# Kernel optimization log

Hardware: AMD Instinct MI355X
Metric: run time of the kernel (lower is better)

## Reference

```python
import jax, jax.numpy as jnp
import numpy as np
import math

D_MODEL = 1024
N_HEADS = 16
D_K = D_MODEL // N_HEADS


def setup_inputs() -> dict:
    key = jax.random.key(0)
    ks = jax.random.split(key, 12)
    B, S, D = 4, 2048, D_MODEL
    scale = 1.0 / math.sqrt(D)
    inp = {
        "q": jax.random.normal(ks[0], (B, S, D), jnp.float32),
        "k": jax.random.normal(ks[1], (B, S, D), jnp.float32),
        "v": jax.random.normal(ks[2], (B, S, D), jnp.float32),
        "w_q": jax.random.normal(ks[3], (D, D), jnp.float32) * scale,
        "b_q": jnp.zeros((D,), jnp.float32),
        "w_k": jax.random.normal(ks[4], (D, D), jnp.float32) * scale,
        "b_k": jnp.zeros((D,), jnp.float32),
        "w_v": jax.random.normal(ks[5], (D, D), jnp.float32) * scale,
        "b_v": jnp.zeros((D,), jnp.float32),
        "w_o": jax.random.normal(ks[6], (D, D), jnp.float32) * scale,
        "b_o": jnp.zeros((D,), jnp.float32),
        "ln_gamma": jnp.ones((D,), jnp.float32),
        "ln_beta": jnp.zeros((D,), jnp.float32),
    }
    return inp


def reference(q, k, v, w_q, b_q, w_k, b_k, w_v, b_v, w_o, b_o, ln_gamma, ln_beta):
    B, Sq, D = q.shape
    Sk = k.shape[1]
    residual = q
    # Projections (torch Linear: x @ W.T + b); split into heads -> [B, H, S, d_k]
    qh = (q @ w_q.T + b_q).reshape(B, Sq, N_HEADS, D_K).transpose(0, 2, 1, 3)
    kh = (k @ w_k.T + b_k).reshape(B, Sk, N_HEADS, D_K).transpose(0, 2, 1, 3)
    vh = (v @ w_v.T + b_v).reshape(B, Sk, N_HEADS, D_K).transpose(0, 2, 1, 3)
    # Scaled dot-product attention (dropout is identity in eval mode)
    scores = jnp.einsum("bhqd,bhkd->bhqk", qh, kh) / jnp.sqrt(jnp.float32(D_K))
    attn = jax.nn.softmax(scores, axis=-1)  # [B, H, Sq, Sk]
    ctx = jnp.einsum("bhqk,bhkd->bhqd", attn, vh)
    ctx = ctx.transpose(0, 2, 1, 3).reshape(B, Sq, D)
    out = ctx @ w_o.T + b_o
    # Post-LN with residual
    x = out + residual
    mu = jnp.mean(x, axis=-1, keepdims=True)
    var = jnp.var(x, axis=-1, keepdims=True)
    out = (x - mu) / jnp.sqrt(var + 1e-5) * ln_gamma + ln_beta
    return out, attn
```

## Files before the change

### kernel.cpp

```cpp
#include <hip/hip_runtime.h>

#define B_ 4
#define S_ 2048
#define D_ 1024
#define H_ 16
#define DK_ 64
#define M_ (B_ * S_)

typedef __attribute__((ext_vector_type(8))) _Float16 f16x8;
typedef __attribute__((ext_vector_type(4))) _Float16 f16x4;
typedef __attribute__((ext_vector_type(4))) float f32x4;

#define QSCALE 0.18033688011113607f

__device__ __forceinline__ f32x4 mfma16(f16x8 a, f16x8 b, f32x4 c) {
  return __builtin_amdgcn_mfma_f32_16x16x32_f16(a, b, c, 0, 0, 0);
}

__device__ __forceinline__ void gl2lds(const _Float16* g, _Float16* l) {
  __builtin_amdgcn_global_load_lds(
      (const __attribute__((address_space(1))) void*)g,
      (__attribute__((address_space(3))) void*)l, 16, 0, 0);
}

#define NW8 (D_ * D_ / 8)
__global__ __launch_bounds__(256) void cvt_w(
    const float* __restrict__ wq, const float* __restrict__ wk,
    const float* __restrict__ wv, const float* __restrict__ wo,
    _Float16* __restrict__ wqh, _Float16* __restrict__ wkh,
    _Float16* __restrict__ wvh, _Float16* __restrict__ woh) {
  const int i = blockIdx.x * 256 + threadIdx.x;
  const int t = i >> 17;
  const int off = i & (NW8 - 1);
  const float* src = t == 0 ? wq : (t == 1 ? wk : (t == 2 ? wv : wo));
  _Float16* dst = t == 0 ? wqh : (t == 1 ? wkh : (t == 2 ? wvh : woh));
  const f32x4 a = *reinterpret_cast<const f32x4*>(&src[(size_t)off * 8]);
  const f32x4 b = *reinterpret_cast<const f32x4*>(&src[(size_t)off * 8 + 4]);
  f16x8 h;
  h[0] = (_Float16)a[0]; h[1] = (_Float16)a[1]; h[2] = (_Float16)a[2]; h[3] = (_Float16)a[3];
  h[4] = (_Float16)b[0]; h[5] = (_Float16)b[1]; h[6] = (_Float16)b[2]; h[7] = (_Float16)b[3];
  *reinterpret_cast<f16x8*>(&dst[(size_t)off * 8]) = h;
}

__global__ __launch_bounds__(256) void gemm_qkv(
    const float* __restrict__ Xq, const float* __restrict__ Xk, const float* __restrict__ Xv,
    const _Float16* __restrict__ Wq, const _Float16* __restrict__ Wk, const _Float16* __restrict__ Wv,
    const float* __restrict__ bq, const float* __restrict__ bk, const float* __restrict__ bv,
    _Float16* __restrict__ Qh, _Float16* __restrict__ Kh, _Float16* __restrict__ Vt) {
  __shared__ _Float16 As[128 * 72];
  __shared__ _Float16 Bs[128 * 64];
  const int third = blockIdx.x >> 9;
  const int bid = blockIdx.x & 511;
  const float* X = third == 0 ? Xq : (third == 1 ? Xk : Xv);
  const _Float16* Bw = third == 0 ? Wq : (third == 1 ? Wk : Wv);
  const float* bias = third == 0 ? bq : (third == 1 ? bk : bv);

  const int t = threadIdx.x;
  const int lane = t & 63;
  const int w = t >> 6;
  const int wr = w >> 1, wc = w & 1;
  const int l15 = lane & 15, g = lane >> 4;
  const int m0 = (bid & 63) * 128;
  const int n0 = (bid >> 6) * 128;

  f32x4 acc[4][4] = {};
  const int srow = lane >> 3;
  const int schk = (lane & 7) * 8;
  const int ar = t >> 4;
  const int ac = (t & 15) * 4;

  for (int kt = 0; kt < 16; ++kt) {
    const int k0 = kt * 64;
#pragma unroll
    for (int u = 0; u < 4; ++u)
      gl2lds(&Bw[(size_t)(n0 + u * 32 + w * 8 + srow) * D_ + k0 + schk], &Bs[u * 2048 + w * 512]);
#pragma unroll
    for (int rg = 0; rg < 8; ++rg) {
      const int r = rg * 16 + ar;
      const f32x4 vv = *reinterpret_cast<const f32x4*>(&X[(size_t)(m0 + r) * D_ + k0 + ac]);
      f16x4 hh;
      hh[0] = (_Float16)vv[0]; hh[1] = (_Float16)vv[1];
      hh[2] = (_Float16)vv[2]; hh[3] = (_Float16)vv[3];
      *reinterpret_cast<f16x4*>(&As[r * 72 + ac]) = hh;
    }
    __syncthreads();
#pragma unroll
    for (int kk = 0; kk < 2; ++kk) {
      f16x8 af[4], bfr[4];
#pragma unroll
      for (int m = 0; m < 4; ++m)
        af[m] = *reinterpret_cast<const f16x8*>(&As[(wr * 64 + m * 16 + l15) * 72 + kk * 32 + 8 * g]);
#pragma unroll
      for (int n = 0; n < 4; ++n)
        bfr[n] = *reinterpret_cast<const f16x8*>(&Bs[(wc * 64 + n * 16 + l15) * 64 + kk * 32 + 8 * g]);
#pragma unroll
      for (int m = 0; m < 4; ++m)
#pragma unroll
        for (int n = 0; n < 4; ++n)
          acc[m][n] = mfma16(af[m], bfr[n], acc[m][n]);
    }
    __syncthreads();
  }

  if (third < 2) {
    _Float16* Y = third == 0 ? Qh : Kh;
    const float scl = third == 0 ? QSCALE : 1.0f;
#pragma unroll
    for (int m = 0; m < 4; ++m)
#pragma unroll
      for (int n = 0; n < 4; ++n)
#pragma unroll
        for (int i = 0; i < 4; ++i) {
          const int R = m0 + wr * 64 + m * 16 + 4 * g + i;
          const int C = n0 + wc * 64 + n * 16 + l15;
          Y[(size_t)R * D_ + C] = (_Float16)((acc[m][n][i] + bias[C]) * scl);
        }
  } else {
#pragma unroll
    for (int m = 0; m < 4; ++m)
#pragma unroll
      for (int n = 0; n < 4; ++n) {
        const int R0 = m0 + wr * 64 + m * 16 + 4 * g;
        const int C = n0 + wc * 64 + n * 16 + l15;
        const int b = R0 >> 11, s0 = R0 & (S_ - 1);
        const int h = C >> 6, dk = C & (DK_ - 1);
        f16x4 hv;
#pragma unroll
        for (int i = 0; i < 4; ++i) hv[i] = (_Float16)(acc[m][n][i] + bias[C]);
        *reinterpret_cast<f16x4*>(&Vt[((size_t)((b * H_ + h) * DK_ + dk)) * S_ + s0]) = hv;
      }
  }
}

__global__ __launch_bounds__(256) void gemm_out(const _Float16* __restrict__ A,
                                                const _Float16* __restrict__ Bw,
                                                const float* __restrict__ bias,
                                                float* __restrict__ out) {
  __shared__ _Float16 As[128 * 64];
  __shared__ _Float16 Bs[128 * 64];
  const int t = threadIdx.x;
  const int lane = t & 63;
  const int w = t >> 6;
  const int wr = w >> 1, wc = w & 1;
  const int l15 = lane & 15, g = lane >> 4;
  const int m0 = (blockIdx.x & 63) * 128;
  const int n0 = (blockIdx.x >> 6) * 128;

  f32x4 acc[4][4] = {};
  const int srow = lane >> 3;
  const int schk = (lane & 7) * 8;

  for (int kt = 0; kt < 16; ++kt) {
    const int k0 = kt * 64;
#pragma unroll
    for (int u = 0; u < 4; ++u) {
      const int r = u * 32 + w * 8 + srow;
      gl2lds(&A[(size_t)(m0 + r) * D_ + k0 + schk], &As[u * 2048 + w * 512]);
      gl2lds(&Bw[(size_t)(n0 + r) * D_ + k0 + schk], &Bs[u * 2048 + w * 512]);
    }
    __syncthreads();
#pragma unroll
    for (int kk = 0; kk < 2; ++kk) {
      f16x8 af[4], bfr[4];
#pragma unroll
      for (int m = 0; m < 4; ++m)
        af[m] = *reinterpret_cast<const f16x8*>(&As[(wr * 64 + m * 16 + l15) * 64 + kk * 32 + 8 * g]);
#pragma unroll
      for (int n = 0; n < 4; ++n)
        bfr[n] = *reinterpret_cast<const f16x8*>(&Bs[(wc * 64 + n * 16 + l15) * 64 + kk * 32 + 8 * g]);
#pragma unroll
      for (int m = 0; m < 4; ++m)
#pragma unroll
        for (int n = 0; n < 4; ++n)
          acc[m][n] = mfma16(af[m], bfr[n], acc[m][n]);
    }
    __syncthreads();
  }

#pragma unroll
  for (int m = 0; m < 4; ++m)
#pragma unroll
    for (int n = 0; n < 4; ++n)
#pragma unroll
      for (int i = 0; i < 4; ++i) {
        const int R = m0 + wr * 64 + m * 16 + 4 * g + i;
        const int C = n0 + wc * 64 + n * 16 + l15;
        out[(size_t)R * D_ + C] = acc[m][n][i] + bias[C];
      }
}

__global__ __launch_bounds__(256) void attn_pass1(const _Float16* __restrict__ Qh,
                                                  const _Float16* __restrict__ Kh,
                                                  float* __restrict__ lbuf) {
  __shared__ float red[4][64];
  const int t = threadIdx.x;
  const int lane = t & 63;
  const int w = t >> 6;
  const int l15 = lane & 15, g = lane >> 4;
  const int qc = blockIdx.x & 31;
  const int bh = blockIdx.x >> 5;
  const int b = bh >> 4, h = bh & 15;
  const int q0 = qc * 64;
  const _Float16* Qp = Qh + (size_t)b * S_ * D_ + h * DK_;
  const _Float16* Kp = Kh + (size_t)b * S_ * D_ + h * DK_;

  f16x8 qa[4][2];
#pragma unroll
  for (int mr = 0; mr < 4; ++mr)
#pragma unroll
    for (int kk = 0; kk < 2; ++kk)
      qa[mr][kk] = *reinterpret_cast<const f16x8*>(&Qp[(size_t)(q0 + mr * 16 + l15) * D_ + kk * 32 + 8 * g]);

  float l[4][4] = {};
  const int cbeg = w * (S_ / 4), cend = cbeg + (S_ / 4);
  for (int c0 = cbeg; c0 < cend; c0 += 16) {
    const f16x8 kb0 = *reinterpret_cast<const f16x8*>(&Kp[(size_t)(c0 + l15) * D_ + 8 * g]);
    const f16x8 kb1 = *reinterpret_cast<const f16x8*>(&Kp[(size_t)(c0 + l15) * D_ + 32 + 8 * g]);
#pragma unroll
    for (int mr = 0; mr < 4; ++mr) {
      f32x4 sc = {};
      sc = mfma16(qa[mr][0], kb0, sc);
      sc = mfma16(qa[mr][1], kb1, sc);
#pragma unroll
      for (int i = 0; i < 4; ++i) l[mr][i] += exp2f(sc[i]);
    }
  }
#pragma unroll
  for (int mask = 1; mask < 16; mask <<= 1)
#pragma unroll
    for (int mr = 0; mr < 4; ++mr)
#pragma unroll
      for (int i = 0; i < 4; ++i) l[mr][i] += __shfl_xor(l[mr][i], mask, 64);
  if (l15 == 0)
#pragma unroll
    for (int mr = 0; mr < 4; ++mr)
#pragma unroll
      for (int i = 0; i < 4; ++i) red[w][mr * 16 + 4 * g + i] = l[mr][i];
  __syncthreads();
  if (t < 64)
    lbuf[(size_t)bh * S_ + q0 + t] = red[0][t] + red[1][t] + red[2][t] + red[3][t];
}

__global__ __launch_bounds__(256) void attn_pass2(const _Float16* __restrict__ Qh,
                                                  const _Float16* __restrict__ Kh,
                                                  const _Float16* __restrict__ Vt,
                                                  const float* __restrict__ lbuf,
                                                  float* __restrict__ attn,
                                                  _Float16* __restrict__ ctx) {
  __shared__ float Ps[4][32 * 36];
  const int t = threadIdx.x;
  const int lane = t & 63;
  const int w = t >> 6;
  const int l15 = lane & 15, g = lane >> 4;
  const int qc = blockIdx.x & 15;
  const int bh = blockIdx.x >> 4;
  const int b = bh >> 4, h = bh & 15;
  const int q0 = qc * 128 + w * 32;
  const _Float16* Qp = Qh + (size_t)b * S_ * D_ + h * DK_;
  const _Float16* Kp = Kh + (size_t)b * S_ * D_ + h * DK_;
  const _Float16* Vp = Vt + (size_t)bh * DK_ * S_;

  f16x8 qa[2][2];
#pragma unroll
  for (int mr = 0; mr < 2; ++mr)
#pragma unroll
    for (int kk = 0; kk < 2; ++kk)
      qa[mr][kk] = *reinterpret_cast<const f16x8*>(&Qp[(size_t)(q0 + mr * 16 + l15) * D_ + kk * 32 + 8 * g]);

  float il[2][4];
#pragma unroll
  for (int mr = 0; mr < 2; ++mr)
#pragma unroll
    for (int i = 0; i < 4; ++i)
      il[mr][i] = 1.0f / lbuf[(size_t)bh * S_ + q0 + mr * 16 + 4 * g + i];

  f32x4 accv[2][4] = {};
  float* Pw = Ps[w];
  const int sr = lane >> 3;
  const int sc4 = (lane & 7) * 4;

  for (int c0 = 0; c0 < S_; c0 += 32) {
#pragma unroll
    for (int ct = 0; ct < 2; ++ct) {
      const f16x8 kb0 = *reinterpret_cast<const f16x8*>(&Kp[(size_t)(c0 + ct * 16 + l15) * D_ + 8 * g]);
      const f16x8 kb1 = *reinterpret_cast<const f16x8*>(&Kp[(size_t)(c0 + ct * 16 + l15) * D_ + 32 + 8 * g]);
#pragma unroll
      for (int mr = 0; mr < 2; ++mr) {
        f32x4 sc = {};
        sc = mfma16(qa[mr][0], kb0, sc);
        sc = mfma16(qa[mr][1], kb1, sc);
#pragma unroll
        for (int i = 0; i < 4; ++i)
          Pw[(mr * 16 + 4 * g + i) * 36 + ct * 16 + l15] = exp2f(sc[i]) * il[mr][i];
      }
    }
#pragma unroll
    for (int j = 0; j < 4; ++j) {
      const int r = sr + 8 * j;
      const f32x4 pv = *reinterpret_cast<const f32x4*>(&Pw[r * 36 + sc4]);
      __builtin_nontemporal_store(pv,
          reinterpret_cast<f32x4*>(&attn[((size_t)bh * S_ + q0 + r) * S_ + c0 + sc4]));
    }
#pragma unroll
    for (int mr = 0; mr < 2; ++mr) {
      const f32x4 p0 = *reinterpret_cast<const f32x4*>(&Pw[(mr * 16 + l15) * 36 + 8 * g]);
      const f32x4 p1 = *reinterpret_cast<const f32x4*>(&Pw[(mr * 16 + l15) * 36 + 8 * g + 4]);
      f16x8 pa;
#pragma unroll
      for (int j = 0; j < 4; ++j) { pa[j] = (_Float16)p0[j]; pa[4 + j] = (_Float16)p1[j]; }
#pragma unroll
      for (int n = 0; n < 4; ++n) {
        const f16x8 vb = *reinterpret_cast<const f16x8*>(&Vp[(size_t)(n * 16 + l15) * S_ + c0 + 8 * g]);
        accv[mr][n] = mfma16(pa, vb, accv[mr][n]);
      }
    }
  }
#pragma unroll
  for (int mr = 0; mr < 2; ++mr)
#pragma unroll
    for (int n = 0; n < 4; ++n)
#pragma unroll
      for (int i = 0; i < 4; ++i) {
        const int row = q0 + mr * 16 + 4 * g + i;
        ctx[((size_t)(b * S_ + row)) * D_ + h * DK_ + n * 16 + l15] = (_Float16)accv[mr][n][i];
      }
}

__global__ __launch_bounds__(256) void ln_kernel(float* __restrict__ out,
                                                 const float* __restrict__ resid,
                                                 const float* __restrict__ gamma,
                                                 const float* __restrict__ beta) {
  __shared__ float red[8];
  const int row = blockIdx.x;
  const int t = threadIdx.x;
  const int lane = t & 63, w = t >> 6;
  const size_t base = (size_t)row * D_ + t * 4;
  const f32x4 o = *reinterpret_cast<const f32x4*>(&out[base]);
  const f32x4 r = *reinterpret_cast<const f32x4*>(&resid[base]);
  const f32x4 x = o + r;
  float s = x[0] + x[1] + x[2] + x[3];
  float s2 = x[0] * x[0] + x[1] * x[1] + x[2] * x[2] + x[3] * x[3];
#pragma unroll
  for (int mask = 1; mask < 64; mask <<= 1) {
    s += __shfl_xor(s, mask, 64);
    s2 += __shfl_xor(s2, mask, 64);
  }
  if (lane == 0) { red[w] = s; red[w + 4] = s2; }
  __syncthreads();
  s = red[0] + red[1] + red[2] + red[3];
  s2 = red[4] + red[5] + red[6] + red[7];
  const float mu = s * (1.0f / D_);
  const float var = s2 * (1.0f / D_) - mu * mu;
  const float rstd = rsqrtf(var + 1e-5f);
  const f32x4 gm = *reinterpret_cast<const f32x4*>(&gamma[t * 4]);
  const f32x4 bt = *reinterpret_cast<const f32x4*>(&beta[t * 4]);
  f32x4 y;
#pragma unroll
  for (int j = 0; j < 4; ++j) y[j] = (x[j] - mu) * rstd * gm[j] + bt[j];
  *reinterpret_cast<f32x4*>(&out[base]) = y;
}

extern "C" void kernel_launch(void* const* d_in, const int* in_sizes, int n_in,
                              void* d_out, int out_size, void* d_ws, size_t ws_size,
                              hipStream_t stream) {
  (void)in_sizes; (void)n_in; (void)out_size; (void)ws_size;
  const float* q    = (const float*)d_in[0];
  const float* k    = (const float*)d_in[1];
  const float* v    = (const float*)d_in[2];
  const float* w_q  = (const float*)d_in[3];
  const float* b_q  = (const float*)d_in[4];
  const float* w_k  = (const float*)d_in[5];
  const float* b_k  = (const float*)d_in[6];
  const float* w_v  = (const float*)d_in[7];
  const float* b_v  = (const float*)d_in[8];
  const float* w_o  = (const float*)d_in[9];
  const float* b_o  = (const float*)d_in[10];
  const float* ln_g = (const float*)d_in[11];
  const float* ln_b = (const float*)d_in[12];

  char* ws = (char*)d_ws;
  _Float16* wq_h = (_Float16*)(ws + ((size_t)0 << 20));
  _Float16* wk_h = (_Float16*)(ws + ((size_t)2 << 20));
  _Float16* wv_h = (_Float16*)(ws + ((size_t)4 << 20));
  _Float16* wo_h = (_Float16*)(ws + ((size_t)6 << 20));
  _Float16* Qh   = (_Float16*)(ws + ((size_t)8 << 20));
  _Float16* Kh   = (_Float16*)(ws + ((size_t)26 << 20));
  _Float16* Vt   = (_Float16*)(ws + ((size_t)44 << 20));
  _Float16* ctx  = (_Float16*)(ws + ((size_t)62 << 20));
  float*    lbuf = (float*)(ws + ((size_t)80 << 20));

  float* out_f = (float*)d_out;
  float* attn_f = out_f + (size_t)M_ * D_;

  cvt_w<<<4 * NW8 / 256, 256, 0, stream>>>(w_q, w_k, w_v, w_o, wq_h, wk_h, wv_h, wo_h);

  gemm_qkv<<<1536, 256, 0, stream>>>(q, k, v, wq_h, wk_h, wv_h, b_q, b_k, b_v, Qh, Kh, Vt);

  attn_pass1<<<B_ * H_ * (S_ / 64), 256, 0, stream>>>(Qh, Kh, lbuf);
  attn_pass2<<<B_ * H_ * (S_ / 128), 256, 0, stream>>>(Qh, Kh, Vt, lbuf, attn_f, ctx);

  gemm_out<<<512, 256, 0, stream>>>(ctx, wo_h, b_o, out_f);
  ln_kernel<<<M_, 256, 0, stream>>>(out_f, q, ln_g, ln_b);
}
```

Baseline: 509.5 us.

## Pre-convert activations to fp16 and use 32x32 MFMA in attention pass 2

The cvt kernel now also converts q, k and v to fp16 ahead of time, so the QKV GEMM can stream both operands into LDS with direct global-to-LDS loads instead of converting fp32 in registers. Attention pass 2 switches from 16x16x32 to 32x32x16 MFMA tiles for both QK^T and PV, which needs fewer instructions and reloads fewer K/V fragments. The cost is an extra full fp32 read and fp16 write of the inputs. The A tile in LDS also loses its row padding, which may introduce bank conflicts.

```diff
diff --git a/kernel.cpp b/kernel.cpp
--- a/kernel.cpp
+++ b/kernel.cpp
@@ -10,11 +10,15 @@
 typedef __attribute__((ext_vector_type(8))) _Float16 f16x8;
 typedef __attribute__((ext_vector_type(4))) _Float16 f16x4;
 typedef __attribute__((ext_vector_type(4))) float f32x4;
+typedef __attribute__((ext_vector_type(16))) float f32x16;
 
 #define QSCALE 0.18033688011113607f
 
 __device__ __forceinline__ f32x4 mfma16(f16x8 a, f16x8 b, f32x4 c) {
   return __builtin_amdgcn_mfma_f32_16x16x32_f16(a, b, c, 0, 0, 0);
+}
+__device__ __forceinline__ f32x16 mfma32(f16x8 a, f16x8 b, f32x16 c) {
+  return __builtin_amdgcn_mfma_f32_32x32x16_f16(a, b, c, 0, 0, 0);
 }
 
 __device__ __forceinline__ void gl2lds(const _Float16* g, _Float16* l) {
@@ -23,17 +27,31 @@
       (__attribute__((address_space(3))) void*)l, 16, 0, 0);
 }
 
+#define NIN8 (M_ * D_ / 8)
 #define NW8 (D_ * D_ / 8)
-__global__ __launch_bounds__(256) void cvt_w(
-    const float* __restrict__ wq, const float* __restrict__ wk,
-    const float* __restrict__ wv, const float* __restrict__ wo,
-    _Float16* __restrict__ wqh, _Float16* __restrict__ wkh,
-    _Float16* __restrict__ wvh, _Float16* __restrict__ woh) {
+__global__ __launch_bounds__(256) void cvt_all(
+    const float* __restrict__ q, const float* __restrict__ k, const float* __restrict__ v,
+    const float* __restrict__ wq, const float* __restrict__ wk, const float* __restrict__ wv,
+    const float* __restrict__ wo,
+    _Float16* __restrict__ qf, _Float16* __restrict__ kf, _Float16* __restrict__ vf,
+    _Float16* __restrict__ wqh, _Float16* __restrict__ wkh, _Float16* __restrict__ wvh,
+    _Float16* __restrict__ woh) {
   const int i = blockIdx.x * 256 + threadIdx.x;
-  const int t = i >> 17;
-  const int off = i & (NW8 - 1);
-  const float* src = t == 0 ? wq : (t == 1 ? wk : (t == 2 ? wv : wo));
-  _Float16* dst = t == 0 ? wqh : (t == 1 ? wkh : (t == 2 ? wvh : woh));
+  const float* src;
+  _Float16* dst;
+  int off;
+  if (i < 3 * NIN8) {
+    const int t = i >> 20;
+    off = i & (NIN8 - 1);
+    src = t == 0 ? q : (t == 1 ? k : v);
+    dst = t == 0 ? qf : (t == 1 ? kf : vf);
+  } else {
+    const int j = i - 3 * NIN8;
+    const int t = j >> 17;
+    off = j & (NW8 - 1);
+    src = t == 0 ? wq : (t == 1 ? wk : (t == 2 ? wv : wo));
+    dst = t == 0 ? wqh : (t == 1 ? wkh : (t == 2 ? wvh : woh));
+  }
   const f32x4 a = *reinterpret_cast<const f32x4*>(&src[(size_t)off * 8]);
   const f32x4 b = *reinterpret_cast<const f32x4*>(&src[(size_t)off * 8 + 4]);
   f16x8 h;
@@ -43,15 +61,15 @@
 }
 
 __global__ __launch_bounds__(256) void gemm_qkv(
-    const float* __restrict__ Xq, const float* __restrict__ Xk, const float* __restrict__ Xv,
+    const _Float16* __restrict__ Aq, const _Float16* __restrict__ Ak, const _Float16* __restrict__ Av,
     const _Float16* __restrict__ Wq, const _Float16* __restrict__ Wk, const _Float16* __restrict__ Wv,
     const float* __restrict__ bq, const float* __restrict__ bk, const float* __restrict__ bv,
     _Float16* __restrict__ Qh, _Float16* __restrict__ Kh, _Float16* __restrict__ Vt) {
-  __shared__ _Float16 As[128 * 72];
+  __shared__ _Float16 As[128 * 64];
   __shared__ _Float16 Bs[128 * 64];
   const int third = blockIdx.x >> 9;
   const int bid = blockIdx.x & 511;
-  const float* X = third == 0 ? Xq : (third == 1 ? Xk : Xv);
+  const _Float16* A = third == 0 ? Aq : (third == 1 ? Ak : Av);
   const _Float16* Bw = third == 0 ? Wq : (third == 1 ? Wk : Wv);
   const float* bias = third == 0 ? bq : (third == 1 ? bk : bv);
 
@@ -66,22 +84,14 @@
   f32x4 acc[4][4] = {};
   const int srow = lane >> 3;
   const int schk = (lane & 7) * 8;
-  const int ar = t >> 4;
-  const int ac = (t & 15) * 4;
 
   for (int kt = 0; kt < 16; ++kt) {
     const int k0 = kt * 64;
 #pragma unroll
-    for (int u = 0; u < 4; ++u)
-      gl2lds(&Bw[(size_t)(n0 + u * 32 + w * 8 + srow) * D_ + k0 + schk], &Bs[u * 2048 + w * 512]);
-#pragma unroll
-    for (int rg = 0; rg < 8; ++rg) {
-      const int r = rg * 16 + ar;
-      const f32x4 vv = *reinterpret_cast<const f32x4*>(&X[(size_t)(m0 + r) * D_ + k0 + ac]);
-      f16x4 hh;
-      hh[0] = (_Float16)vv[0]; hh[1] = (_Float16)vv[1];
-      hh[2] = (_Float16)vv[2]; hh[3] = (_Float16)vv[3];
-      *reinterpret_cast<f16x4*>(&As[r * 72 + ac]) = hh;
+    for (int u = 0; u < 4; ++u) {
+      const int r = u * 32 + w * 8 + srow;
+      gl2lds(&A[(size_t)(m0 + r) * D_ + k0 + schk], &As[u * 2048 + w * 512]);
+      gl2lds(&Bw[(size_t)(n0 + r) * D_ + k0 + schk], &Bs[u * 2048 + w * 512]);
     }
     __syncthreads();
 #pragma unroll
@@ -89,7 +99,7 @@
       f16x8 af[4], bfr[4];
 #pragma unroll
       for (int m = 0; m < 4; ++m)
-        af[m] = *reinterpret_cast<const f16x8*>(&As[(wr * 64 + m * 16 + l15) * 72 + kk * 32 + 8 * g]);
+        af[m] = *reinterpret_cast<const f16x8*>(&As[(wr * 64 + m * 16 + l15) * 64 + kk * 32 + 8 * g]);
 #pragma unroll
       for (int n = 0; n < 4; ++n)
         bfr[n] = *reinterpret_cast<const f16x8*>(&Bs[(wc * 64 + n * 16 + l15) * 64 + kk * 32 + 8 * g]);
@@ -251,7 +261,7 @@
   const int t = threadIdx.x;
   const int lane = t & 63;
   const int w = t >> 6;
-  const int l15 = lane & 15, g = lane >> 4;
+  const int l31 = lane & 31, hs = lane >> 5;
   const int qc = blockIdx.x & 15;
   const int bh = blockIdx.x >> 4;
   const int b = bh >> 4, h = bh & 15;
@@ -260,70 +270,59 @@
   const _Float16* Kp = Kh + (size_t)b * S_ * D_ + h * DK_;
   const _Float16* Vp = Vt + (size_t)bh * DK_ * S_;
 
-  f16x8 qa[2][2];
-#pragma unroll
-  for (int mr = 0; mr < 2; ++mr)
-#pragma unroll
-    for (int kk = 0; kk < 2; ++kk)
-      qa[mr][kk] = *reinterpret_cast<const f16x8*>(&Qp[(size_t)(q0 + mr * 16 + l15) * D_ + kk * 32 + 8 * g]);
-
-  float il[2][4];
-#pragma unroll
-  for (int mr = 0; mr < 2; ++mr)
-#pragma unroll
-    for (int i = 0; i < 4; ++i)
-      il[mr][i] = 1.0f / lbuf[(size_t)bh * S_ + q0 + mr * 16 + 4 * g + i];
-
-  f32x4 accv[2][4] = {};
+  f16x8 qa[4];
+#pragma unroll
+  for (int kc = 0; kc < 4; ++kc)
+    qa[kc] = *reinterpret_cast<const f16x8*>(&Qp[(size_t)(q0 + l31) * D_ + kc * 16 + 8 * hs]);
+
+  float il[16];
+#pragma unroll
+  for (int r = 0; r < 16; ++r)
+    il[r] = 1.0f / lbuf[(size_t)bh * S_ + q0 + (r & 3) + 8 * (r >> 2) + 4 * hs];
+
+  f32x16 pv0 = {}, pv1 = {};
   float* Pw = Ps[w];
   const int sr = lane >> 3;
   const int sc4 = (lane & 7) * 4;
 
   for (int c0 = 0; c0 < S_; c0 += 32) {
-#pragma unroll
-    for (int ct = 0; ct < 2; ++ct) {
-      const f16x8 kb0 = *reinterpret_cast<const f16x8*>(&Kp[(size_t)(c0 + ct * 16 + l15) * D_ + 8 * g]);
-      const f16x8 kb1 = *reinterpret_cast<const f16x8*>(&Kp[(size_t)(c0 + ct * 16 + l15) * D_ + 32 + 8 * g]);
-#pragma unroll
-      for (int mr = 0; mr < 2; ++mr) {
-        f32x4 sc = {};
-        sc = mfma16(qa[mr][0], kb0, sc);
-        sc = mfma16(qa[mr][1], kb1, sc);
-#pragma unroll
-        for (int i = 0; i < 4; ++i)
-          Pw[(mr * 16 + 4 * g + i) * 36 + ct * 16 + l15] = exp2f(sc[i]) * il[mr][i];
-      }
-    }
+    f32x16 sc = {};
+#pragma unroll
+    for (int kc = 0; kc < 4; ++kc) {
+      const f16x8 kb = *reinterpret_cast<const f16x8*>(&Kp[(size_t)(c0 + l31) * D_ + kc * 16 + 8 * hs]);
+      sc = mfma32(qa[kc], kb, sc);
+    }
+#pragma unroll
+    for (int r = 0; r < 16; ++r)
+      Pw[((r & 3) + 8 * (r >> 2) + 4 * hs) * 36 + l31] = exp2f(sc[r]) * il[r];
 #pragma unroll
     for (int j = 0; j < 4; ++j) {
       const int r = sr + 8 * j;
-      const f32x4 pv = *reinterpret_cast<const f32x4*>(&Pw[r * 36 + sc4]);
-      __builtin_nontemporal_store(pv,
+      const f32x4 pvv = *reinterpret_cast<const f32x4*>(&Pw[r * 36 + sc4]);
+      __builtin_nontemporal_store(pvv,
           reinterpret_cast<f32x4*>(&attn[((size_t)bh * S_ + q0 + r) * S_ + c0 + sc4]));
     }
 #pragma unroll
-    for (int mr = 0; mr < 2; ++mr) {
-      const f32x4 p0 = *reinterpret_cast<const f32x4*>(&Pw[(mr * 16 + l15) * 36 + 8 * g]);
-      const f32x4 p1 = *reinterpret_cast<const f32x4*>(&Pw[(mr * 16 + l15) * 36 + 8 * g + 4]);
+    for (int kc2 = 0; kc2 < 2; ++kc2) {
+      const int cb = kc2 * 16 + 8 * hs;
+      const f32x4 p0 = *reinterpret_cast<const f32x4*>(&Pw[l31 * 36 + cb]);
+      const f32x4 p1 = *reinterpret_cast<const f32x4*>(&Pw[l31 * 36 + cb + 4]);
       f16x8 pa;
 #pragma unroll
-      for (int j = 0; j < 4; ++j) { pa[j] = (_Float16)p0[j]; pa[4 + j] = (_Float16)p1[j]; }
-#pragma unroll
-      for (int n = 0; n < 4; ++n) {
-        const f16x8 vb = *reinterpret_cast<const f16x8*>(&Vp[(size_t)(n * 16 + l15) * S_ + c0 + 8 * g]);
-        accv[mr][n] = mfma16(pa, vb, accv[mr][n]);
-      }
-    }
-  }
-#pragma unroll
-  for (int mr = 0; mr < 2; ++mr)
-#pragma unroll
-    for (int n = 0; n < 4; ++n)
-#pragma unroll
-      for (int i = 0; i < 4; ++i) {
-        const int row = q0 + mr * 16 + 4 * g + i;
-        ctx[((size_t)(b * S_ + row)) * D_ + h * DK_ + n * 16 + l15] = (_Float16)accv[mr][n][i];
-      }
+      for (int jj = 0; jj < 4; ++jj) { pa[jj] = (_Float16)p0[jj]; pa[4 + jj] = (_Float16)p1[jj]; }
+      const f16x8 vb0 = *reinterpret_cast<const f16x8*>(&Vp[(size_t)(0 * 32 + l31) * S_ + c0 + cb]);
+      const f16x8 vb1 = *reinterpret_cast<const f16x8*>(&Vp[(size_t)(1 * 32 + l31) * S_ + c0 + cb]);
+      pv0 = mfma32(pa, vb0, pv0);
+      pv1 = mfma32(pa, vb1, pv1);
+    }
+  }
+#pragma unroll
+  for (int r = 0; r < 16; ++r) {
+    const int row = q0 + (r & 3) + 8 * (r >> 2) + 4 * hs;
+    _Float16* cp = &ctx[((size_t)(b * S_ + row)) * D_ + h * DK_];
+    cp[l31] = (_Float16)pv0[r];
+    cp[32 + l31] = (_Float16)pv1[r];
+  }
 }
 
 __global__ __launch_bounds__(256) void ln_kernel(float* __restrict__ out,
@@ -383,18 +382,22 @@
   _Float16* wk_h = (_Float16*)(ws + ((size_t)2 << 20));
   _Float16* wv_h = (_Float16*)(ws + ((size_t)4 << 20));
   _Float16* wo_h = (_Float16*)(ws + ((size_t)6 << 20));
-  _Float16* Qh   = (_Float16*)(ws + ((size_t)8 << 20));
-  _Float16* Kh   = (_Float16*)(ws + ((size_t)26 << 20));
-  _Float16* Vt   = (_Float16*)(ws + ((size_t)44 << 20));
-  _Float16* ctx  = (_Float16*)(ws + ((size_t)62 << 20));
-  float*    lbuf = (float*)(ws + ((size_t)80 << 20));
+  _Float16* qf   = (_Float16*)(ws + ((size_t)8 << 20));
+  _Float16* kf   = (_Float16*)(ws + ((size_t)26 << 20));
+  _Float16* vf   = (_Float16*)(ws + ((size_t)44 << 20));
+  _Float16* Qh   = (_Float16*)(ws + ((size_t)62 << 20));
+  _Float16* Kh   = (_Float16*)(ws + ((size_t)80 << 20));
+  _Float16* Vt   = (_Float16*)(ws + ((size_t)98 << 20));
+  _Float16* ctx  = (_Float16*)(ws + ((size_t)116 << 20));
+  float*    lbuf = (float*)(ws + ((size_t)134 << 20));
 
   float* out_f = (float*)d_out;
   float* attn_f = out_f + (size_t)M_ * D_;
 
-  cvt_w<<<4 * NW8 / 256, 256, 0, stream>>>(w_q, w_k, w_v, w_o, wq_h, wk_h, wv_h, wo_h);
-
-  gemm_qkv<<<1536, 256, 0, stream>>>(q, k, v, wq_h, wk_h, wv_h, b_q, b_k, b_v, Qh, Kh, Vt);
+  cvt_all<<<(3 * NIN8 + 4 * NW8) / 256, 256, 0, stream>>>(
+      q, k, v, w_q, w_k, w_v, w_o, qf, kf, vf, wq_h, wk_h, wv_h, wo_h);
+
+  gemm_qkv<<<1536, 256, 0, stream>>>(qf, kf, vf, wq_h, wk_h, wv_h, b_q, b_k, b_v, Qh, Kh, Vt);
 
   attn_pass1<<<B_ * H_ * (S_ / 64), 256, 0, stream>>>(Qh, Kh, lbuf);
   attn_pass2<<<B_ * H_ * (S_ / 128), 256, 0, stream>>>(Qh, Kh, Vt, lbuf, attn_f, ctx);
```

Measured after the change: 528.2 us. +3.7%, slower.
